# Performance work log

Hardware: AMD Instinct MI355X
Metric: run time of the kernel (lower is better)

Reference implementation:

```python
import jax, jax.numpy as jnp
import numpy as np
from jax import lax

INIT_STRIDE = 10.0
COARSE_STRIDE = 4.0
DOWN_SAMPLE = 4.0
NUM_POINT = 128
N_INST = 2000


def setup_inputs() -> dict:
    key = jax.random.key(0)
    ks = jax.random.split(key, 12)
    B, C, H, W = 4, 64, 256, 256
    return {
        'cnn_feature': jax.random.normal(ks[0], (B, C, H, W), jnp.float32),
        'wh_pred': jax.random.normal(ks[1], (B, NUM_POINT * 2, H, W), jnp.float32),
        'ct_ind': jax.random.randint(ks[2], (N_INST,), 0, H * W, jnp.int64 if jax.config.jax_enable_x64 else jnp.int32),
        'ct_img_idx': jax.random.randint(ks[3], (N_INST,), 0, B, jnp.int64 if jax.config.jax_enable_x64 else jnp.int32),
        'conv1_w': jax.random.normal(ks[4], (256, 64, 3, 3), jnp.float32) * 0.05,
        'conv1_b': jax.random.normal(ks[5], (256,), jnp.float32) * 0.05,
        'conv2_w': jax.random.normal(ks[6], (64, 256, 1, 1), jnp.float32) * 0.05,
        'conv2_b': jax.random.normal(ks[7], (64,), jnp.float32) * 0.05,
        'w_poly': jax.random.normal(ks[8], (NUM_POINT * 4, (NUM_POINT + 1) * 64), jnp.float32) * 0.02,
        'w_fuse': jax.random.normal(ks[9], (NUM_POINT * 2, NUM_POINT * 4), jnp.float32) * 0.02,
        'b_fuse': jax.random.normal(ks[10], (NUM_POINT * 2,), jnp.float32) * 0.02,
    }


def bilinear_sample(feat, pts, img_idx):
    # feat [B,C,H,W]; pts [N,P,2] pixel coords; img_idx [N]
    # matches torch grid_sample(align_corners=False, padding_mode='zeros')
    # with grid = pts/(WH/2) - 1  =>  sample coord = pts - 0.5
    B, C, H, W = feat.shape
    sx = pts[..., 0] - 0.5
    sy = pts[..., 1] - 0.5
    x0 = jnp.floor(sx).astype(jnp.int32); x1 = x0 + 1
    y0 = jnp.floor(sy).astype(jnp.int32); y1 = y0 + 1
    wx1 = sx - x0; wx0 = 1.0 - wx1
    wy1 = sy - y0; wy0 = 1.0 - wy1
    bidx = img_idx[:, None].astype(jnp.int32)  # [N,1]

    def corner(yc, xc, w):
        valid = (xc >= 0) & (xc < W) & (yc >= 0) & (yc < H)
        g = feat[bidx, :, jnp.clip(yc, 0, H - 1), jnp.clip(xc, 0, W - 1)]  # [N,P,C]
        return g * (w * valid)[..., None]

    out = (corner(y0, x0, wy0 * wx0) + corner(y0, x1, wy0 * wx1)
           + corner(y1, x0, wy1 * wx0) + corner(y1, x1, wy1 * wx1))
    return out  # [N,P,C]


def _forward(cnn_feature, wh_pred, ct_ind, ct_img_idx, conv1_w, conv1_b, conv2_w, conv2_b, w_poly, w_fuse, b_fuse):
    B, Cf, H, W = cnn_feature.shape
    N = ct_ind.shape[0]
    ct_x = jnp.clip(ct_ind % W, 0, W - 1)
    ct_y = jnp.clip(ct_ind // W, 0, H - 1)
    # gather polygon offsets at center locations: [N, 2*P] -> [N, P, 2]
    ct_offset = wh_pred[ct_img_idx, :, ct_y, ct_x].reshape(N, NUM_POINT, 2)
    ct = jnp.stack([ct_x, ct_y], axis=1).astype(jnp.float32)  # [N,2]
    init_polys = ct_offset * INIT_STRIDE + ct[:, None, :]  # [N,P,2]

    # Refine.trans_feature: conv3x3(64->256)+ReLU -> conv1x1(256->64)
    dn = ('NCHW', 'OIHW', 'NCHW')
    f = lax.conv_general_dilated(cnn_feature, conv1_w, (1, 1), 'SAME', dimension_numbers=dn) + conv1_b[None, :, None, None]
    f = jax.nn.relu(f)
    f = lax.conv_general_dilated(f, conv2_w, (1, 1), 'VALID', dimension_numbers=dn) + conv2_b[None, :, None, None]

    points = jnp.concatenate([ct[:, None, :], init_polys], axis=1)  # [N,P+1,2]
    fp = bilinear_sample(f, points, ct_img_idx)  # [N,P+1,64]
    fp = fp.transpose(0, 2, 1).reshape(N, -1)  # [N, 64*(P+1)] (C-major like torch)

    off = fp @ w_poly.T            # trans_poly (no bias)
    off = off @ w_fuse.T + b_fuse  # trans_fuse
    off = off.reshape(N, NUM_POINT, 2)
    coarse_polys = off * COARSE_STRIDE + lax.stop_gradient(init_polys)
    # stacked outputs: poly_init*down, poly_coarse*down -> [2,N,P,2]
    return jnp.stack([init_polys * DOWN_SAMPLE, coarse_polys * DOWN_SAMPLE])


def reference(cnn_feature, wh_pred, ct_ind, ct_img_idx, conv1_w, conv1_b, conv2_w, conv2_b, w_poly, w_fuse, b_fuse):
    return _forward(cnn_feature, wh_pred, ct_ind, ct_img_idx, conv1_w, conv1_b, conv2_w, conv2_b, w_poly, w_fuse, b_fuse)
```

## Files before the change

kernel.cpp:

```cpp
#include <hip/hip_runtime.h>

typedef unsigned short ushort_t;
typedef __bf16 bf16x8 __attribute__((ext_vector_type(8)));
typedef float f32x4 __attribute__((ext_vector_type(4)));

__device__ __forceinline__ ushort_t f2b(float f) {
  union { float f; unsigned u; } v; v.f = f;
  unsigned r = v.u + 0x7FFFu + ((v.u >> 16) & 1u);
  return (ushort_t)(r >> 16);
}
__device__ __forceinline__ float b2f(ushort_t u) {
  union { unsigned u; float f; } v; v.u = ((unsigned)u) << 16;
  return v.f;
}
__device__ __forceinline__ f32x4 MFMA(bf16x8 a, bf16x8 b, f32x4 c) {
  return __builtin_amdgcn_mfma_f32_16x16x32_bf16(a, b, c, 0, 0, 0);
}
__device__ __forceinline__ void gload_lds16(const ushort_t* g, ushort_t* l) {
  __builtin_amdgcn_global_load_lds(
      (const __attribute__((address_space(1))) unsigned int*)g,
      (__attribute__((address_space(3))) unsigned int*)l, 16, 0, 0);
}

#define XTW 258

__global__ void zero_border_kernel(ushort_t* __restrict__ xt) {
  int i = blockIdx.x * 256 + threadIdx.x;
  if (i >= 32896) return;
  int px_id = i >> 3, oct = (i & 7) << 3;
  int img = px_id / 1028, r = px_id - img * 1028;
  int row, col;
  if (r < 516) { row = (r < 258) ? 0 : 257; col = (r < 258) ? r : r - 258; }
  else { int rr = r - 516; row = 1 + (rr >> 1); col = (rr & 1) ? 257 : 0; }
  uint4 z = make_uint4(0, 0, 0, 0);
  *(uint4*)(xt + (((size_t)img * XTW + row) * XTW + col) * 64 + oct) = z;
}

__global__ void cast_xt_kernel(const float* __restrict__ x, ushort_t* __restrict__ xt) {
  __shared__ float tile[64][65];
  int blk = blockIdx.x;
  int b = blk >> 10, rest = blk & 1023;
  int y = rest >> 2, xseg = (rest & 3) << 6;
  int p0 = y * 256 + xseg;
  int t = threadIdx.x;
#pragma unroll
  for (int rep = 0; rep < 16; ++rep) {
    int lin = rep * 256 + t;
    int c = lin >> 6, p = lin & 63;
    tile[c][p] = x[((size_t)(b * 64 + c)) * 65536 + p0 + p];
  }
  __syncthreads();
#pragma unroll
  for (int rep = 0; rep < 2; ++rep) {
    int u = rep * 256 + t;
    int p = u >> 3, cc = (u & 7) << 3;
    union { ushort_t s[8]; uint4 v; } pk;
#pragma unroll
    for (int j = 0; j < 8; ++j) pk.s[j] = f2b(tile[cc + j][p]);
    int gx = xseg + p + 1;
    size_t base = (((size_t)b * XTW + (y + 1)) * XTW + gx) * 64;
    *(uint4*)(xt + base + (cc ^ ((gx & 7) << 3))) = pk.v;
  }
}

__global__ void cast_w1t_kernel(const float* __restrict__ w1, ushort_t* __restrict__ w1t) {
  int i = blockIdx.x * 256 + threadIdx.x;
  int tap = i >> 14;
  int rem = i & 16383;
  int nn = rem >> 6, c = rem & 63;
  int cs = c ^ ((nn & 7) << 3);
  w1t[tap * 16384 + nn * 64 + cs] = f2b(w1[(nn * 64 + c) * 9 + tap]);
}

__global__ void cast_f32_bf16_kernel(const float* __restrict__ src, ushort_t* __restrict__ dst, int n) {
  for (int i = blockIdx.x * blockDim.x + threadIdx.x; i < n; i += gridDim.x * blockDim.x)
    dst[i] = f2b(src[i]);
}

__global__ void cast_wp_kernel(const float* __restrict__ src, ushort_t* __restrict__ dst) {
  for (int i = blockIdx.x * blockDim.x + threadIdx.x; i < 4227072; i += gridDim.x * blockDim.x) {
    int row = i / 8256;
    int col = i - row * 8256;
    dst[row * 8256 + (col ^ ((row & 7) << 3))] = f2b(src[i]);
  }
}

__global__ void prep_kernel(const float* __restrict__ wh, const int* __restrict__ ct_ind,
                            const int* __restrict__ ct_b, float* __restrict__ out,
                            float* __restrict__ pts) {
  int n = blockIdx.x, t = threadIdx.x;
  int ci = ct_ind[n];
  int b = ct_b[n];
  int ctx = ci & 255;
  int cty = (ci >> 8) & 255;
  float fx = (float)ctx, fy = (float)cty;
  size_t base = ((size_t)b * 256 + 2 * t) * 65536 + (size_t)cty * 256 + ctx;
  float ox = wh[base];
  float oy = wh[base + 65536];
  float ix = ox * 10.f + fx, iy = oy * 10.f + fy;
  out[(n * 128 + t) * 2]     = ix * 4.f;
  out[(n * 128 + t) * 2 + 1] = iy * 4.f;
  float* pn = pts + (size_t)n * 258;
  if (t == 0) { pn[0] = fx; pn[1] = fy; }
  pn[2 + t * 2] = ix;
  pn[3 + t * 2] = iy;
}

__global__ __launch_bounds__(512, 1)
void conv_fused_kernel(const ushort_t* __restrict__ xt, const ushort_t* __restrict__ w1t,
                       const float* __restrict__ b1, const float* __restrict__ w2,
                       const float* __restrict__ b2, ushort_t* __restrict__ f2) {
  __shared__ __align__(16) char smem[163840];
  ushort_t* strip = (ushort_t*)smem;
  ushort_t* Bb0   = (ushort_t*)(smem + 69632);
  ushort_t* Bb1   = (ushort_t*)(smem + 102400);
  ushort_t* F1    = (ushort_t*)smem;
  ushort_t* W2l   = (ushort_t*)(smem + 131072);
  ushort_t* T     = (ushort_t*)smem;

  int rawblk = blockIdx.x;
  int blk = ((rawblk & 7) << 7) + (rawblk >> 3);
  int b = blk >> 8;
  int rest = blk & 255;
  int y2 = (rest >> 1) << 1;
  int x0 = (rest & 1) << 7;
  int tid = threadIdx.x;
  int wid = tid >> 6, lane = tid & 63;
  int l15 = lane & 15, lg = lane >> 4;
  int wm = (wid >> 1) << 6;
  int wn = (wid & 1) << 7;

#pragma unroll
  for (int j = 0; j < 4; ++j) {
    int q = (wid << 2) + j;
    gload_lds16(w1t + q * 512 + lane * 8, Bb0 + q * 512);
  }
#pragma unroll
  for (int j = 0; j < 4; ++j) {
    int q = (wid << 2) + j;
    gload_lds16(w1t + 16384 + q * 512 + lane * 8, Bb1 + q * 512);
  }
  for (int c = wid; c < 68; c += 8) {
    int ry = c / 17, ck = c - ry * 17;
    const ushort_t* g = xt + (((size_t)b * XTW + (y2 + ry)) * XTW + x0 + ck * 8) * 64 + lane * 8;
    gload_lds16(g, strip + (ry * 136 + ck * 8) * 64);
  }
  asm volatile("s_waitcnt vmcnt(0) lgkmcnt(0)" ::: "memory");
  asm volatile("s_barrier" ::: "memory");

  f32x4 acc[4][8] = {};

#pragma unroll
  for (int tap = 0; tap < 9; ++tap) {
    const int dy = tap / 3 - 1, dx = tap % 3 - 1;
    ushort_t* Bcur = (tap & 1) ? Bb1 : Bb0;
    if (tap < 8) {
      ushort_t* Bnxt = (tap & 1) ? Bb0 : Bb1;
      const ushort_t* gb = w1t + (tap + 1) * 16384;
#pragma unroll
      for (int j = 0; j < 4; ++j) {
        int q = (wid << 2) + j;
        gload_lds16(gb + q * 512 + lane * 8, Bnxt + q * 512);
      }
    }
    const int sr  = (wm >> 7) + dy + 1;
    const int spb = (wm & 127) + dx + 1;
#pragma unroll
    for (int kk = 0; kk < 2; ++kk) {
      int c0 = (kk << 5) + (lg << 3);
      bf16x8 a[4];
#pragma unroll
      for (int m = 0; m < 4; ++m) {
        int sp = spb + m * 16 + l15;
        a[m] = *(const bf16x8*)(strip + ((sr * 136 + sp) << 6) + (c0 ^ ((sp & 7) << 3)));
      }
#pragma unroll
      for (int nf = 0; nf < 8; ++nf) {
        int br = wn + nf * 16 + l15;
        bf16x8 bb = *(const bf16x8*)(Bcur + (br << 6) + (c0 ^ ((br & 7) << 3)));
#pragma unroll
        for (int m = 0; m < 4; ++m)
          acc[m][nf] = MFMA(a[m], bb, acc[m][nf]);
      }
    }
    if (tap < 8) {
      asm volatile("s_waitcnt vmcnt(0)" ::: "memory");
      asm volatile("s_barrier" ::: "memory");
    }
  }
  __syncthreads();

#pragma unroll
  for (int nf = 0; nf < 8; ++nf) {
    int ch = wn + nf * 16 + l15;
    float bias = b1[ch];
#pragma unroll
    for (int m = 0; m < 4; ++m) {
#pragma unroll
      for (int r = 0; r < 4; ++r) {
        int p = wm + m * 16 + lg * 4 + r;
        F1[(p << 8) + (ch ^ ((p & 7) << 3))] = f2b(fmaxf(acc[m][nf][r] + bias, 0.f));
      }
    }
  }
#pragma unroll
  for (int it = 0; it < 4; ++it) {
    int u = it * 512 + tid;
    int oc = u >> 5, ic = (u & 31) << 3;
    float4 fa = *(const float4*)(w2 + (oc << 8) + ic);
    float4 fb = *(const float4*)(w2 + (oc << 8) + ic + 4);
    union { ushort_t s[8]; uint4 v; } pk;
    pk.s[0] = f2b(fa.x); pk.s[1] = f2b(fa.y); pk.s[2] = f2b(fa.z); pk.s[3] = f2b(fa.w);
    pk.s[4] = f2b(fb.x); pk.s[5] = f2b(fb.y); pk.s[6] = f2b(fb.z); pk.s[7] = f2b(fb.w);
    *(uint4*)(W2l + (oc << 8) + (ic ^ ((oc & 7) << 3))) = pk.v;
  }
  __syncthreads();
  int wpx = wid << 5;
  f32x4 acc2[2][4] = {};
#pragma unroll
  for (int kc = 0; kc < 8; ++kc) {
    int c0 = (kc << 5) + (lg << 3);
    bf16x8 a2[2];
#pragma unroll
    for (int mm = 0; mm < 2; ++mm) {
      int p = wpx + mm * 16 + l15;
      a2[mm] = *(const bf16x8*)(F1 + (p << 8) + (c0 ^ ((p & 7) << 3)));
    }
#pragma unroll
    for (int nf = 0; nf < 4; ++nf) {
      int oc = nf * 16 + l15;
      bf16x8 bw = *(const bf16x8*)(W2l + (oc << 8) + (c0 ^ ((oc & 7) << 3)));
#pragma unroll
      for (int mm = 0; mm < 2; ++mm)
        acc2[mm][nf] = MFMA(a2[mm], bw, acc2[mm][nf]);
    }
  }
  __syncthreads();
#pragma unroll
  for (int mm = 0; mm < 2; ++mm)
#pragma unroll
    for (int nf = 0; nf < 4; ++nf) {
      int oc = nf * 16 + l15;
      float bias = b2[oc];
#pragma unroll
      for (int r = 0; r < 4; ++r) {
        int p = wpx + mm * 16 + lg * 4 + r;
        T[(p << 6) + (oc ^ ((p & 7) << 3))] = f2b(acc2[mm][nf][r] + bias);
      }
    }
  __syncthreads();
  const size_t imgbase = (size_t)b * 65536;
#pragma unroll
  for (int it = 0; it < 4; ++it) {
    int u = it * 512 + tid;
    int p = u >> 3, co = (u & 7) << 3;
    uint4 v = *(const uint4*)(T + (p << 6) + (co ^ ((p & 7) << 3)));
    int gpx = (y2 + (p >> 7)) * 256 + x0 + (p & 127);
    *(uint4*)(f2 + (imgbase + gpx) * 64 + co) = v;
  }
}

__global__ void sample_kernel(const ushort_t* __restrict__ f2, const float* __restrict__ pts,
                              const int* __restrict__ ct_b, ushort_t* __restrict__ fp) {
  int n = blockIdx.x, t = threadIdx.x;
  __shared__ float pl[258];
  __shared__ __align__(16) ushort_t fpl[8256];
  int b = ct_b[n];
  const ushort_t* fb = f2 + (size_t)b * 4194304;
  for (int i = t; i < 258; i += 128) pl[i] = pts[(size_t)n * 258 + i];
  __syncthreads();
  int c4 = t & 15;
  int ps = t >> 4;
  for (int base = 0; base < 136; base += 8) {
    int pt = base + ps;
    bool live = pt < 129;
    int ptc = live ? pt : 0;
    float px = pl[ptc * 2], py = pl[ptc * 2 + 1];
    float sx = px - 0.5f, sy = py - 0.5f;
    float fx0 = floorf(sx), fy0 = floorf(sy);
    int x0 = (int)fx0, y0 = (int)fy0;
    float wx1 = sx - fx0, wy1 = sy - fy0;
    float wx0 = 1.f - wx1, wy0 = 1.f - wy1;
    float a0 = 0.f, a1 = 0.f, a2 = 0.f, a3 = 0.f;
#pragma unroll
    for (int cy = 0; cy < 2; ++cy) {
#pragma unroll
      for (int cx = 0; cx < 2; ++cx) {
        int yc = y0 + cy, xc = x0 + cx;
        float w = (cy ? wy1 : wy0) * (cx ? wx1 : wx0);
        bool valid = (xc >= 0) && (xc < 256) && (yc >= 0) && (yc < 256);
        int ycc = min(max(yc, 0), 255), xcc = min(max(xc, 0), 255);
        uint2 v = *(const uint2*)(fb + ((size_t)(ycc * 256 + xcc)) * 64 + (c4 << 2));
        float ww = valid ? w : 0.f;
        a0 += b2f((ushort_t)(v.x & 0xFFFF)) * ww;
        a1 += b2f((ushort_t)(v.x >> 16)) * ww;
        a2 += b2f((ushort_t)(v.y & 0xFFFF)) * ww;
        a3 += b2f((ushort_t)(v.y >> 16)) * ww;
      }
    }
    if (live) {
      int ch = c4 << 2;
      fpl[(ch + 0) * 129 + pt] = f2b(a0);
      fpl[(ch + 1) * 129 + pt] = f2b(a1);
      fpl[(ch + 2) * 129 + pt] = f2b(a2);
      fpl[(ch + 3) * 129 + pt] = f2b(a3);
    }
  }
  __syncthreads();
  uint4* fo = (uint4*)(fp + (size_t)n * 8256);
  const uint4* fi = (const uint4*)fpl;
  int key = n & 7;
  for (int i = t; i < 1032; i += 128) fo[i ^ key] = fi[i];
}

__global__ __launch_bounds__(256)
void gemm_splitk_kernel(const ushort_t* __restrict__ A, const ushort_t* __restrict__ B,
                        float* __restrict__ partials) {
  __shared__ __align__(16) ushort_t Al[8192];
  __shared__ __align__(16) ushort_t Bl[8192];
  int spatial = blockIdx.x;
  int kc = blockIdx.y;
  int n_t = (spatial & 7) >> 1;
  int m_t = ((spatial >> 3) << 1) | (spatial & 1);
  int m0 = m_t << 7, n0 = n_t << 7;
  int ks0 = (129 * kc) >> 3, ks1 = (129 * (kc + 1)) >> 3;

  int tid = threadIdx.x;
  int wid = tid >> 6, lane = tid & 63;
  int l15 = lane & 15, lg = lane >> 4;
  int wm = (wid >> 1) << 6, wn = (wid & 1) << 6;
  int srow = (lane >> 3);
  int soct = lane & 7;
  f32x4 acc[4][4] = {};
  for (int ks = ks0; ks < ks1; ++ks) {
    __syncthreads();
#pragma unroll
    for (int j = 0; j < 4; ++j) {
      int q = (wid << 2) + j;
      int r = (q << 3) + srow;
      int ar = m0 + r;
      if (ar >= 2000) ar = 1992 + (ar & 7);
      gload_lds16(A + (size_t)ar * 8256 + ks * 64 + soct * 8, Al + q * 512);
      gload_lds16(B + (size_t)(n0 + r) * 8256 + ks * 64 + soct * 8, Bl + q * 512);
    }
    __syncthreads();
#pragma unroll
    for (int kk = 0; kk < 2; ++kk) {
      int c0 = (kk << 5) + (lg << 3);
      bf16x8 a[4], b[4];
#pragma unroll
      for (int m = 0; m < 4; ++m) {
        int row = wm + m * 16 + l15;
        a[m] = *(const bf16x8*)(Al + (row << 6) + (c0 ^ ((row & 7) << 3)));
      }
#pragma unroll
      for (int nf = 0; nf < 4; ++nf) {
        int row = wn + nf * 16 + l15;
        b[nf] = *(const bf16x8*)(Bl + (row << 6) + (c0 ^ ((row & 7) << 3)));
      }
#pragma unroll
      for (int m = 0; m < 4; ++m)
#pragma unroll
        for (int nf = 0; nf < 4; ++nf)
          acc[m][nf] = MFMA(a[m], b[nf], acc[m][nf]);
    }
  }
  float* pout = partials + (size_t)kc * 1048576;
#pragma unroll
  for (int m = 0; m < 4; ++m)
#pragma unroll
    for (int nf = 0; nf < 4; ++nf)
#pragma unroll
      for (int r = 0; r < 4; ++r) {
        int row = m0 + wm + m * 16 + lg * 4 + r;
        int col = n0 + wn + nf * 16 + l15;
        pout[(size_t)row * 512 + col] = acc[m][nf][r];
      }
}

__global__ void reduce_splitk_kernel(const float* __restrict__ partials,
                                     ushort_t* __restrict__ off1) {
  int i = blockIdx.x * 256 + threadIdx.x;
  size_t idx = (size_t)i * 4;
  float4 s = *(const float4*)(partials + idx);
#pragma unroll
  for (int c = 1; c < 8; ++c) {
    float4 p = *(const float4*)(partials + (size_t)c * 1048576 + idx);
    s.x += p.x; s.y += p.y; s.z += p.z; s.w += p.w;
  }
  union { ushort_t u[4]; uint2 v; } pk;
  pk.u[0] = f2b(s.x); pk.u[1] = f2b(s.y); pk.u[2] = f2b(s.z); pk.u[3] = f2b(s.w);
  *(uint2*)(off1 + idx) = pk.v;
}

__global__ __launch_bounds__(256)
void gemm64_epi_kernel(const ushort_t* __restrict__ A, const ushort_t* __restrict__ B,
                       const float* __restrict__ bias, const float* __restrict__ out0,
                       float* __restrict__ out1, int Mvalid) {
  __shared__ ushort_t Alds[64][72];
  __shared__ ushort_t Blds[64][72];
  const int K = 512;
  int n0 = blockIdx.x * 64, m0 = blockIdx.y * 64;
  int tid = threadIdx.x;
  int wid = tid >> 6, lane = tid & 63;
  int l15 = lane & 15, lg = lane >> 4;
  int wm = (wid >> 1) * 32, wn = (wid & 1) * 32;
  f32x4 acc[2][2] = {};
  for (int ks = 0; ks < K / 64; ++ks) {
    __syncthreads();
#pragma unroll
    for (int it = 0; it < 2; ++it) {
      int u = it * 256 + tid;
      int r = u >> 3, cc = (u & 7) << 3;
      *(uint4*)(&Alds[r][cc]) = *(const uint4*)(A + (size_t)(m0 + r) * K + ks * 64 + cc);
      *(uint4*)(&Blds[r][cc]) = *(const uint4*)(B + (size_t)(n0 + r) * K + ks * 64 + cc);
    }
    __syncthreads();
#pragma unroll
    for (int kk = 0; kk < 2; ++kk) {
      int c0 = (kk << 5) + (lg << 3);
      bf16x8 a[2], b[2];
      a[0] = *(const bf16x8*)(&Alds[wm + l15][c0]);
      a[1] = *(const bf16x8*)(&Alds[wm + 16 + l15][c0]);
      b[0] = *(const bf16x8*)(&Blds[wn + l15][c0]);
      b[1] = *(const bf16x8*)(&Blds[wn + 16 + l15][c0]);
#pragma unroll
      for (int m = 0; m < 2; ++m)
#pragma unroll
        for (int nf = 0; nf < 2; ++nf)
          acc[m][nf] = MFMA(a[m], b[nf], acc[m][nf]);
    }
  }
#pragma unroll
  for (int m = 0; m < 2; ++m)
#pragma unroll
    for (int nf = 0; nf < 2; ++nf)
#pragma unroll
      for (int r = 0; r < 4; ++r) {
        int row = m0 + wm + m * 16 + lg * 4 + r;
        int col = n0 + wn + nf * 16 + l15;
        if (row < Mvalid) {
          float v = acc[m][nf][r] + bias[col];
          out1[(size_t)row * 256 + col] = v * 16.f + out0[(size_t)row * 256 + col];
        }
      }
}

extern "C" void kernel_launch(void* const* d_in, const int* in_sizes, int n_in,
                              void* d_out, int out_size, void* d_ws, size_t ws_size,
                              hipStream_t stream) {
  const float* x    = (const float*)d_in[0];
  const float* wh   = (const float*)d_in[1];
  const int* ct_ind = (const int*)d_in[2];
  const int* ct_b   = (const int*)d_in[3];
  const float* w1   = (const float*)d_in[4];
  const float* b1   = (const float*)d_in[5];
  const float* w2   = (const float*)d_in[6];
  const float* b2   = (const float*)d_in[7];
  const float* wp   = (const float*)d_in[8];
  const float* wf   = (const float*)d_in[9];
  const float* bfu  = (const float*)d_in[10];
  float* out = (float*)d_out;
  char* ws = (char*)d_ws;

  ushort_t* xt    = (ushort_t*)(ws + 0);
  float* partials = (float*)(ws + 0);
  ushort_t* w1t   = (ushort_t*)(ws + 34080768);
  ushort_t* f2    = (ushort_t*)(ws + 34375680);
  ushort_t* wpb   = (ushort_t*)(ws + 67930112);
  ushort_t* wfb   = (ushort_t*)(ws + 76384256);
  ushort_t* fp    = (ushort_t*)(ws + 76646400);
  ushort_t* off1  = (ushort_t*)(ws + 109670400);
  float*    pts   = (float*)(ws + 111767552);

  zero_border_kernel<<<dim3(129), dim3(256), 0, stream>>>(xt);
  cast_xt_kernel<<<dim3(4096), dim3(256), 0, stream>>>(x, xt);
  cast_w1t_kernel<<<dim3(576), dim3(256), 0, stream>>>(w1, w1t);
  cast_wp_kernel<<<dim3(2064), dim3(256), 0, stream>>>(wp, wpb);
  cast_f32_bf16_kernel<<<dim3(64), dim3(256), 0, stream>>>(wf, wfb, 131072);
  prep_kernel<<<dim3(2000), dim3(128), 0, stream>>>(wh, ct_ind, ct_b, out, pts);
  conv_fused_kernel<<<dim3(1024), dim3(512), 0, stream>>>(xt, w1t, b1, w2, b2, f2);
  sample_kernel<<<dim3(2000), dim3(128), 0, stream>>>(f2, pts, ct_b, fp);
  gemm_splitk_kernel<<<dim3(64, 8), dim3(256), 0, stream>>>(fp, wpb, partials);
  reduce_splitk_kernel<<<dim3(1024), dim3(256), 0, stream>>>(partials, off1);
  gemm64_epi_kernel<<<dim3(4, 32), dim3(256), 0, stream>>>(off1, wfb, bfu, out,
                                                           out + 512000, 2000);
}
```

Measured before the change: 221.4 us.

## Merge setup kernels into fewer launches and store split-K partials as bf16

The zero-border pass is folded into the activation cast kernel, and the weight casts plus the prep step are combined into one setup kernel. This cuts the launch count from six to two. Split-K GEMM partials are now written as bf16 instead of fp32, which halves the partial-sum traffic written by the GEMM and read back by the reduction. The reduction now reads 8 bf16 values per thread with half the blocks. The cost is extra rounding of each partial before summation, which can lower the accuracy of the intermediate offsets.

```diff
diff --git a/kernel.cpp b/kernel.cpp
--- a/kernel.cpp
+++ b/kernel.cpp
@@ -24,25 +24,26 @@
 
 #define XTW 258
 
-__global__ void zero_border_kernel(ushort_t* __restrict__ xt) {
-  int i = blockIdx.x * 256 + threadIdx.x;
-  if (i >= 32896) return;
-  int px_id = i >> 3, oct = (i & 7) << 3;
-  int img = px_id / 1028, r = px_id - img * 1028;
-  int row, col;
-  if (r < 516) { row = (r < 258) ? 0 : 257; col = (r < 258) ? r : r - 258; }
-  else { int rr = r - 516; row = 1 + (rr >> 1); col = (rr & 1) ? 257 : 0; }
-  uint4 z = make_uint4(0, 0, 0, 0);
-  *(uint4*)(xt + (((size_t)img * XTW + row) * XTW + col) * 64 + oct) = z;
-}
-
 __global__ void cast_xt_kernel(const float* __restrict__ x, ushort_t* __restrict__ xt) {
   __shared__ float tile[64][65];
   int blk = blockIdx.x;
+  int t = threadIdx.x;
+  if (blk >= 4096) {
+    int i = (blk - 4096) * 256 + t;
+    if (i < 32896) {
+      int px_id = i >> 3, oct = (i & 7) << 3;
+      int img = px_id / 1028, r = px_id - img * 1028;
+      int row, col;
+      if (r < 516) { row = (r < 258) ? 0 : 257; col = (r < 258) ? r : r - 258; }
+      else { int rr = r - 516; row = 1 + (rr >> 1); col = (rr & 1) ? 257 : 0; }
+      uint4 z = make_uint4(0, 0, 0, 0);
+      *(uint4*)(xt + (((size_t)img * XTW + row) * XTW + col) * 64 + oct) = z;
+    }
+    return;
+  }
   int b = blk >> 10, rest = blk & 1023;
   int y = rest >> 2, xseg = (rest & 3) << 6;
   int p0 = y * 256 + xseg;
-  int t = threadIdx.x;
 #pragma unroll
   for (int rep = 0; rep < 16; ++rep) {
     int lin = rep * 256 + t;
@@ -63,47 +64,48 @@
   }
 }
 
-__global__ void cast_w1t_kernel(const float* __restrict__ w1, ushort_t* __restrict__ w1t) {
-  int i = blockIdx.x * 256 + threadIdx.x;
-  int tap = i >> 14;
-  int rem = i & 16383;
-  int nn = rem >> 6, c = rem & 63;
-  int cs = c ^ ((nn & 7) << 3);
-  w1t[tap * 16384 + nn * 64 + cs] = f2b(w1[(nn * 64 + c) * 9 + tap]);
-}
-
-__global__ void cast_f32_bf16_kernel(const float* __restrict__ src, ushort_t* __restrict__ dst, int n) {
-  for (int i = blockIdx.x * blockDim.x + threadIdx.x; i < n; i += gridDim.x * blockDim.x)
-    dst[i] = f2b(src[i]);
-}
-
-__global__ void cast_wp_kernel(const float* __restrict__ src, ushort_t* __restrict__ dst) {
-  for (int i = blockIdx.x * blockDim.x + threadIdx.x; i < 4227072; i += gridDim.x * blockDim.x) {
-    int row = i / 8256;
-    int col = i - row * 8256;
-    dst[row * 8256 + (col ^ ((row & 7) << 3))] = f2b(src[i]);
-  }
-}
-
-__global__ void prep_kernel(const float* __restrict__ wh, const int* __restrict__ ct_ind,
-                            const int* __restrict__ ct_b, float* __restrict__ out,
-                            float* __restrict__ pts) {
-  int n = blockIdx.x, t = threadIdx.x;
-  int ci = ct_ind[n];
-  int b = ct_b[n];
-  int ctx = ci & 255;
-  int cty = (ci >> 8) & 255;
-  float fx = (float)ctx, fy = (float)cty;
-  size_t base = ((size_t)b * 256 + 2 * t) * 65536 + (size_t)cty * 256 + ctx;
-  float ox = wh[base];
-  float oy = wh[base + 65536];
-  float ix = ox * 10.f + fx, iy = oy * 10.f + fy;
-  out[(n * 128 + t) * 2]     = ix * 4.f;
-  out[(n * 128 + t) * 2 + 1] = iy * 4.f;
-  float* pn = pts + (size_t)n * 258;
-  if (t == 0) { pn[0] = fx; pn[1] = fy; }
-  pn[2 + t * 2] = ix;
-  pn[3 + t * 2] = iy;
+__global__ void setup_kernel(const float* __restrict__ w1, ushort_t* __restrict__ w1t,
+                             const float* __restrict__ wp, ushort_t* __restrict__ wpb,
+                             const float* __restrict__ wf, ushort_t* __restrict__ wfb,
+                             const float* __restrict__ wh, const int* __restrict__ ct_ind,
+                             const int* __restrict__ ct_b, float* __restrict__ out,
+                             float* __restrict__ pts) {
+  int blk = blockIdx.x, t = threadIdx.x;
+  if (blk < 576) {
+    int i = blk * 256 + t;
+    int tap = i >> 14;
+    int rem = i & 16383;
+    int nn = rem >> 6, c = rem & 63;
+    int cs = c ^ ((nn & 7) << 3);
+    w1t[tap * 16384 + nn * 64 + cs] = f2b(w1[(nn * 64 + c) * 9 + tap]);
+  } else if (blk < 2640) {
+    for (int i = (blk - 576) * 256 + t; i < 4227072; i += 2064 * 256) {
+      int row = i / 8256;
+      int col = i - row * 8256;
+      wpb[row * 8256 + (col ^ ((row & 7) << 3))] = f2b(wp[i]);
+    }
+  } else if (blk < 2704) {
+    for (int i = (blk - 2640) * 256 + t; i < 131072; i += 64 * 256)
+      wfb[i] = f2b(wf[i]);
+  } else {
+    int n = (blk - 2704) * 2 + (t >> 7);
+    int t7 = t & 127;
+    int ci = ct_ind[n];
+    int b = ct_b[n];
+    int ctx = ci & 255;
+    int cty = (ci >> 8) & 255;
+    float fx = (float)ctx, fy = (float)cty;
+    size_t base = ((size_t)b * 256 + 2 * t7) * 65536 + (size_t)cty * 256 + ctx;
+    float ox = wh[base];
+    float oy = wh[base + 65536];
+    float ix = ox * 10.f + fx, iy = oy * 10.f + fy;
+    out[(n * 128 + t7) * 2]     = ix * 4.f;
+    out[(n * 128 + t7) * 2 + 1] = iy * 4.f;
+    float* pn = pts + (size_t)n * 258;
+    if (t7 == 0) { pn[0] = fx; pn[1] = fy; }
+    pn[2 + t7 * 2] = ix;
+    pn[3 + t7 * 2] = iy;
+  }
 }
 
 __global__ __launch_bounds__(512, 1)
@@ -315,7 +317,7 @@
 
 __global__ __launch_bounds__(256)
 void gemm_splitk_kernel(const ushort_t* __restrict__ A, const ushort_t* __restrict__ B,
-                        float* __restrict__ partials) {
+                        ushort_t* __restrict__ partials) {
   __shared__ __align__(16) ushort_t Al[8192];
   __shared__ __align__(16) ushort_t Bl[8192];
   int spatial = blockIdx.x;
@@ -365,7 +367,7 @@
           acc[m][nf] = MFMA(a[m], b[nf], acc[m][nf]);
     }
   }
-  float* pout = partials + (size_t)kc * 1048576;
+  ushort_t* pout = partials + (size_t)kc * 1048576;
 #pragma unroll
   for (int m = 0; m < 4; ++m)
 #pragma unroll
@@ -374,23 +376,27 @@
       for (int r = 0; r < 4; ++r) {
         int row = m0 + wm + m * 16 + lg * 4 + r;
         int col = n0 + wn + nf * 16 + l15;
-        pout[(size_t)row * 512 + col] = acc[m][nf][r];
-      }
-}
-
-__global__ void reduce_splitk_kernel(const float* __restrict__ partials,
+        pout[(size_t)row * 512 + col] = f2b(acc[m][nf][r]);
+      }
+}
+
+__global__ void reduce_splitk_kernel(const ushort_t* __restrict__ partials,
                                      ushort_t* __restrict__ off1) {
   int i = blockIdx.x * 256 + threadIdx.x;
-  size_t idx = (size_t)i * 4;
-  float4 s = *(const float4*)(partials + idx);
-#pragma unroll
-  for (int c = 1; c < 8; ++c) {
-    float4 p = *(const float4*)(partials + (size_t)c * 1048576 + idx);
-    s.x += p.x; s.y += p.y; s.z += p.z; s.w += p.w;
-  }
-  union { ushort_t u[4]; uint2 v; } pk;
-  pk.u[0] = f2b(s.x); pk.u[1] = f2b(s.y); pk.u[2] = f2b(s.z); pk.u[3] = f2b(s.w);
-  *(uint2*)(off1 + idx) = pk.v;
+  size_t idx = (size_t)i * 8;
+  float s[8] = {0.f, 0.f, 0.f, 0.f, 0.f, 0.f, 0.f, 0.f};
+#pragma unroll
+  for (int c = 0; c < 8; ++c) {
+    uint4 v = *(const uint4*)(partials + (size_t)c * 1048576 + idx);
+    s[0] += b2f((ushort_t)(v.x & 0xFFFF)); s[1] += b2f((ushort_t)(v.x >> 16));
+    s[2] += b2f((ushort_t)(v.y & 0xFFFF)); s[3] += b2f((ushort_t)(v.y >> 16));
+    s[4] += b2f((ushort_t)(v.z & 0xFFFF)); s[5] += b2f((ushort_t)(v.z >> 16));
+    s[6] += b2f((ushort_t)(v.w & 0xFFFF)); s[7] += b2f((ushort_t)(v.w >> 16));
+  }
+  union { ushort_t u[8]; uint4 v; } pk;
+#pragma unroll
+  for (int j = 0; j < 8; ++j) pk.u[j] = f2b(s[j]);
+  *(uint4*)(off1 + idx) = pk.v;
 }
 
 __global__ __launch_bounds__(256)
@@ -463,8 +469,8 @@
   float* out = (float*)d_out;
   char* ws = (char*)d_ws;
 
-  ushort_t* xt    = (ushort_t*)(ws + 0);
-  float* partials = (float*)(ws + 0);
+  ushort_t* xt       = (ushort_t*)(ws + 0);
+  ushort_t* partials = (ushort_t*)(ws + 0);
   ushort_t* w1t   = (ushort_t*)(ws + 34080768);
   ushort_t* f2    = (ushort_t*)(ws + 34375680);
   ushort_t* wpb   = (ushort_t*)(ws + 67930112);
@@ -473,16 +479,13 @@
   ushort_t* off1  = (ushort_t*)(ws + 109670400);
   float*    pts   = (float*)(ws + 111767552);
 
-  zero_border_kernel<<<dim3(129), dim3(256), 0, stream>>>(xt);
-  cast_xt_kernel<<<dim3(4096), dim3(256), 0, stream>>>(x, xt);
-  cast_w1t_kernel<<<dim3(576), dim3(256), 0, stream>>>(w1, w1t);
-  cast_wp_kernel<<<dim3(2064), dim3(256), 0, stream>>>(wp, wpb);
-  cast_f32_bf16_kernel<<<dim3(64), dim3(256), 0, stream>>>(wf, wfb, 131072);
-  prep_kernel<<<dim3(2000), dim3(128), 0, stream>>>(wh, ct_ind, ct_b, out, pts);
+  cast_xt_kernel<<<dim3(4225), dim3(256), 0, stream>>>(x, xt);
+  setup_kernel<<<dim3(3704), dim3(256), 0, stream>>>(w1, w1t, wp, wpb, wf, wfb,
+                                                     wh, ct_ind, ct_b, out, pts);
   conv_fused_kernel<<<dim3(1024), dim3(512), 0, stream>>>(xt, w1t, b1, w2, b2, f2);
   sample_kernel<<<dim3(2000), dim3(128), 0, stream>>>(f2, pts, ct_b, fp);
   gemm_splitk_kernel<<<dim3(64, 8), dim3(256), 0, stream>>>(fp, wpb, partials);
-  reduce_splitk_kernel<<<dim3(1024), dim3(256), 0, stream>>>(partials, off1);
+  reduce_splitk_kernel<<<dim3(512), dim3(256), 0, stream>>>(partials, off1);
   gemm64_epi_kernel<<<dim3(4, 32), dim3(256), 0, stream>>>(off1, wfb, bfu, out,
                                                            out + 512000, 2000);
 }
```

New measurement: 200.1 us. 9.6% less time.
